# Performance work log

Measured on AMD Instinct MI355X. Metric: run time of the kernel, lower is better.

The kernel has to match this reference:

```python
import jax, jax.numpy as jnp
import numpy as np

D_MODEL = 2048
NUM_HEADS = 16
HEAD_DIM = D_MODEL // NUM_HEADS
EPS = 1e-6


def setup_inputs() -> dict:
    key = jax.random.key(0)
    ks = jax.random.split(key, 5)
    B, S = 1, 4096
    scale = 1.0 / np.sqrt(D_MODEL)
    return {
        "x": jax.random.normal(ks[0], (B, S, D_MODEL), dtype=jnp.float32),
        "wq": jax.random.normal(ks[1], (D_MODEL, D_MODEL), dtype=jnp.float32) * scale,
        "wk": jax.random.normal(ks[2], (D_MODEL, D_MODEL), dtype=jnp.float32) * scale,
        "wv": jax.random.normal(ks[3], (D_MODEL, D_MODEL), dtype=jnp.float32) * scale,
        "wo": jax.random.normal(ks[4], (D_MODEL, D_MODEL), dtype=jnp.float32) * scale,
        "q_norm_w": jnp.ones((HEAD_DIM,), dtype=jnp.float32),
        "k_norm_w": jnp.ones((HEAD_DIM,), dtype=jnp.float32),
    }


def _rmsnorm(x, w):
    rms = jnp.sqrt(jnp.mean(x * x, axis=-1, keepdims=True) + EPS)
    return x / rms * w


def reference(x, wq, wk, wv, wo, q_norm_w, k_norm_w):
    B, S, _ = x.shape
    # nn.Linear: y = x @ W.T ; split heads -> [B, H, S, Dh]
    def proj(w):
        return (x @ w.T).reshape(B, S, NUM_HEADS, HEAD_DIM).transpose(0, 2, 1, 3)
    q = _rmsnorm(proj(wq), q_norm_w)
    k = _rmsnorm(proj(wk), k_norm_w)
    v = proj(wv)
    scale = 1.0 / np.sqrt(HEAD_DIM)
    attn = jnp.einsum("bhqd,bhkd->bhqk", q, k) * scale  # [B,H,S,S]
    attn = jax.nn.softmax(attn, axis=-1)
    out = jnp.einsum("bhqk,bhkd->bhqd", attn, v)
    out = out.transpose(0, 2, 1, 3).reshape(B, S, D_MODEL)
    return out @ wo.T
```

## Files before the change

kernel.cpp:

```cpp
#include <hip/hip_runtime.h>
#include <hip/hip_bf16.h>

#define S 4096
#define D 2048
#define NH 16
#define HD 128

typedef __attribute__((ext_vector_type(8))) short bf16x8;
typedef __attribute__((ext_vector_type(4))) float f32x4;

typedef __attribute__((address_space(1))) char glob_char;
typedef __attribute__((address_space(3))) char lds_char_t;

__device__ __forceinline__ void gld16(const void* g, void* l) {
    __builtin_amdgcn_global_load_lds((const glob_char*)g, (lds_char_t*)l, 16, 0, 0);
}

__device__ __forceinline__ unsigned short f2b(float f) {
    union { float f; unsigned u; } c; c.f = f;
    unsigned r = c.u + 0x7fff + ((c.u >> 16) & 1);
    return (unsigned short)(r >> 16);
}

__device__ __forceinline__ float fexp2(float x) {
#if __has_builtin(__builtin_amdgcn_exp2f)
    return __builtin_amdgcn_exp2f(x);
#else
    return __expf(x * 0.6931471805599453f);
#endif
}

#define MFMA16(a, b, c) __builtin_amdgcn_mfma_f32_16x16x32_bf16((a), (b), (c), 0, 0, 0)

__global__ __launch_bounds__(256) void cvt_all(
    const float* __restrict__ x,  const float* __restrict__ wq,
    const float* __restrict__ wk, const float* __restrict__ wv,
    const float* __restrict__ wo,
    unsigned short* __restrict__ xb, unsigned short* __restrict__ wqkvb,
    unsigned short* __restrict__ wob)
{
    const int z = blockIdx.y;
    const float* src; unsigned short* dst; int n4;
    if (z == 0)      { src = x;  dst = xb;                        n4 = (S * D) / 4; }
    else if (z == 1) { src = wq; dst = wqkvb;                     n4 = (D * D) / 4; }
    else if (z == 2) { src = wk; dst = wqkvb + (size_t)D * D;     n4 = (D * D) / 4; }
    else if (z == 3) { src = wv; dst = wqkvb + 2 * (size_t)D * D; n4 = (D * D) / 4; }
    else             { src = wo; dst = wob;                       n4 = (D * D) / 4; }
    int i = blockIdx.x * 256 + threadIdx.x;
    if (i < n4) {
        float4 v = ((const float4*)src)[i];
        ushort4 o;
        o.x = f2b(v.x); o.y = f2b(v.y); o.z = f2b(v.z); o.w = f2b(v.w);
        ((ushort4*)dst)[i] = o;
    }
}

template<int OUTMODE>
__global__ __launch_bounds__(512, 2) void gemm8(
    const unsigned short* __restrict__ A, const unsigned short* __restrict__ B,
    void* __restrict__ O0, void* __restrict__ O1, void* __restrict__ O2,
    const float* __restrict__ qw, const float* __restrict__ kw)
{
    __shared__ short lds[65536];
    __shared__ float red[4][256];

    const int tid = threadIdx.x;
    const int lane = tid & 63, col = lane & 15, quad = lane >> 4;
    const int w = tid >> 6, wr = w >> 2, wc = w & 3;

    const int nwg = gridDim.x * gridDim.y;
    const int orig = blockIdx.y * gridDim.x + blockIdx.x;
    const int lin = (orig & 7) * (nwg >> 3) + (orig >> 3);
    const int m0 = (lin / gridDim.x) * 256;
    const int n0 = (lin % gridDim.x) * 256;

    const int srow = tid >> 3;
    const int sslot = (tid & 7) ^ (srow & 7);
    const unsigned short* pa0 = A + (size_t)(m0 + srow) * 2048 + sslot * 8;
    const unsigned short* pb0 = B + (size_t)(n0 + srow) * 2048 + sslot * 8;
    const int dst0 = tid * 8;

    auto stA = [&](int t, int h, int buf) {
        const unsigned short* g = pa0 + (size_t)h * 262144 + t * 64;
        short* d = &lds[buf * 16384 + h * 8192 + dst0];
        gld16(g, d);
        gld16(g + 131072, d + 4096);
    };
    auto stB = [&](int t, int h, int buf) {
        const unsigned short* g = pb0 + (size_t)h * 262144 + t * 64;
        short* d = &lds[32768 + buf * 16384 + h * 8192 + dst0];
        gld16(g, d);
        gld16(g + 131072, d + 4096);
    };

    const int sl0 = (quad ^ (col & 7)) << 3;
    const int arow = (wr * 128 + col) * 64;
    const int brow = (wc * 64 + col) * 64;
    auto rdA = [&](int mf, int kk, int buf) -> bf16x8 {
        return *(const bf16x8*)&lds[buf * 16384 + arow + mf * 1024 + (sl0 ^ (kk << 5))];
    };
    auto rdB = [&](int nf, int kk, int buf) -> bf16x8 {
        return *(const bf16x8*)&lds[32768 + buf * 16384 + brow + nf * 1024 + (sl0 ^ (kk << 5))];
    };

    f32x4 acc[8][4];
    #pragma unroll
    for (int i = 0; i < 8; ++i)
        #pragma unroll
        for (int j = 0; j < 4; ++j)
            #pragma unroll
            for (int r = 0; r < 4; ++r) acc[i][j][r] = 0.0f;

    auto ktile = [&](int buf, int tst, int mode) {
        bf16x8 a0[4][2], a1[4][2], b0[2][2], b1[2][2];
        #pragma unroll
        for (int mf = 0; mf < 4; ++mf) { a0[mf][0] = rdA(mf, 0, buf); a0[mf][1] = rdA(mf, 1, buf); }
        #pragma unroll
        for (int nf = 0; nf < 2; ++nf) { b0[nf][0] = rdB(nf, 0, buf); b0[nf][1] = rdB(nf, 1, buf); }
        __builtin_amdgcn_s_barrier();
        __builtin_amdgcn_s_setprio(1);
        #pragma unroll
        for (int mf = 0; mf < 4; ++mf)
            #pragma unroll
            for (int nf = 0; nf < 2; ++nf) {
                acc[mf][nf] = MFMA16(a0[mf][0], b0[nf][0], acc[mf][nf]);
                acc[mf][nf] = MFMA16(a0[mf][1], b0[nf][1], acc[mf][nf]);
            }
        __builtin_amdgcn_s_setprio(0);
        __builtin_amdgcn_s_barrier();

        #pragma unroll
        for (int mf = 0; mf < 4; ++mf) { a1[mf][0] = rdA(mf + 4, 0, buf); a1[mf][1] = rdA(mf + 4, 1, buf); }
        __builtin_amdgcn_s_barrier();
        __builtin_amdgcn_s_setprio(1);
        #pragma unroll
        for (int mf = 0; mf < 4; ++mf)
            #pragma unroll
            for (int nf = 0; nf < 2; ++nf) {
                acc[mf + 4][nf] = MFMA16(a1[mf][0], b0[nf][0], acc[mf + 4][nf]);
                acc[mf + 4][nf] = MFMA16(a1[mf][1], b0[nf][1], acc[mf + 4][nf]);
            }
        __builtin_amdgcn_s_setprio(0);
        __builtin_amdgcn_s_barrier();

        #pragma unroll
        for (int nf = 0; nf < 2; ++nf) { b1[nf][0] = rdB(nf + 2, 0, buf); b1[nf][1] = rdB(nf + 2, 1, buf); }
        if (mode == 0) { stA(tst, 0, buf); stA(tst, 1, buf); }
        __builtin_amdgcn_s_barrier();
        __builtin_amdgcn_s_setprio(1);
        #pragma unroll
        for (int mf = 0; mf < 4; ++mf)
            #pragma unroll
            for (int nf = 0; nf < 2; ++nf) {
                acc[mf][nf + 2] = MFMA16(a0[mf][0], b1[nf][0], acc[mf][nf + 2]);
                acc[mf][nf + 2] = MFMA16(a0[mf][1], b1[nf][1], acc[mf][nf + 2]);
            }
        __builtin_amdgcn_s_setprio(0);
        __builtin_amdgcn_s_barrier();

        if (mode == 0) { stB(tst, 0, buf); stB(tst, 1, buf); }
        __builtin_amdgcn_s_barrier();
        __builtin_amdgcn_s_setprio(1);
        #pragma unroll
        for (int mf = 0; mf < 4; ++mf)
            #pragma unroll
            for (int nf = 0; nf < 2; ++nf) {
                acc[mf + 4][nf + 2] = MFMA16(a1[mf][0], b1[nf][0], acc[mf + 4][nf + 2]);
                acc[mf + 4][nf + 2] = MFMA16(a1[mf][1], b1[nf][1], acc[mf + 4][nf + 2]);
            }
        __builtin_amdgcn_s_setprio(0);
        if (mode == 0)      asm volatile("s_waitcnt vmcnt(8)" ::: "memory");
        else if (mode == 1) asm volatile("s_waitcnt vmcnt(0)" ::: "memory");
        __builtin_amdgcn_s_barrier();
    };

    stA(0, 0, 0); stA(0, 1, 0); stB(0, 0, 0); stB(0, 1, 0);
    stA(1, 0, 1); stA(1, 1, 1); stB(1, 0, 1); stB(1, 1, 1);
    asm volatile("s_waitcnt vmcnt(8)" ::: "memory");
    __builtin_amdgcn_s_barrier();

    for (int kt = 0; kt < 16; ++kt) {
        const int t0 = kt << 1;
        const bool st = kt < 15;
        ktile(0, t0 + 2, st ? 0 : 1);
        ktile(1, t0 + 3, st ? 0 : 2);
    }

    if (OUTMODE == 1) {
        float* C = (float*)O0;
        #pragma unroll
        for (int mf = 0; mf < 8; ++mf)
            #pragma unroll
            for (int nf = 0; nf < 4; ++nf)
                #pragma unroll
                for (int r = 0; r < 4; ++r)
                    C[(size_t)(m0 + wr * 128 + mf * 16 + quad * 4 + r) * 2048 +
                      n0 + wc * 64 + nf * 16 + col] = acc[mf][nf][r];
    } else {
        const int sel = n0 >> 11;
        if (sel == 2) {
            unsigned short* VtO = (unsigned short*)O2;
            #pragma unroll
            for (int mf = 0; mf < 8; ++mf)
                #pragma unroll
                for (int nf = 0; nf < 4; ++nf) {
                    int n = (n0 & 2047) + wc * 64 + nf * 16 + col;
                    int hh = n >> 7, dv = n & 127;
                    ushort4 pk;
                    pk.x = f2b(acc[mf][nf][0]); pk.y = f2b(acc[mf][nf][1]);
                    pk.z = f2b(acc[mf][nf][2]); pk.w = f2b(acc[mf][nf][3]);
                    *(ushort4*)&VtO[(size_t)hh * (HD * S) + (size_t)dv * S +
                                    m0 + wr * 128 + mf * 16 + quad * 4] = pk;
                }
        } else {
            unsigned short* C = (unsigned short*)(sel == 0 ? O0 : O1);
            const float* wgt = (sel == 0) ? qw : kw;
            const float extra = (sel == 0)
                ? 0.08838834764831845f * 1.4426950408889634f : 1.0f;
            float wv4[4];
            #pragma unroll
            for (int nf = 0; nf < 4; ++nf)
                wv4[nf] = wgt[(wc & 1) * 64 + nf * 16 + col];
            #pragma unroll
            for (int mf = 0; mf < 8; ++mf)
                #pragma unroll
                for (int r = 0; r < 4; ++r) {
                    float ss = 0.0f;
                    #pragma unroll
                    for (int nf = 0; nf < 4; ++nf) ss += acc[mf][nf][r] * acc[mf][nf][r];
                    #pragma unroll
                    for (int d = 1; d < 16; d <<= 1) ss += __shfl_xor(ss, d, 64);
                    if (col == 0) red[wc][wr * 128 + mf * 16 + quad * 4 + r] = ss;
                }
            __syncthreads();
            #pragma unroll
            for (int mf = 0; mf < 8; ++mf) {
                float rsc[4];
                #pragma unroll
                for (int r = 0; r < 4; ++r) {
                    int idx = wr * 128 + mf * 16 + quad * 4 + r;
                    float tot = red[wc & 6][idx] + red[(wc & 6) + 1][idx];
                    rsc[r] = rsqrtf(tot * (1.0f / HD) + 1e-6f) * extra;
                }
                #pragma unroll
                for (int nf = 0; nf < 4; ++nf)
                    #pragma unroll
                    for (int r = 0; r < 4; ++r)
                        C[(size_t)(m0 + wr * 128 + mf * 16 + quad * 4 + r) * 2048 +
                          (n0 & 2047) + wc * 64 + nf * 16 + col] =
                            f2b(acc[mf][nf][r] * rsc[r] * wv4[nf]);
            }
        }
    }
}

struct FlashSmem {
    short Ks[2][8192];
    short Vs[2][8192];
    short Ps[8192];
};

__global__ __launch_bounds__(256, 2) void flash_mfma(
    const unsigned short* __restrict__ Qg, const unsigned short* __restrict__ Kg,
    const unsigned short* __restrict__ Vt, unsigned short* __restrict__ Ctx)
{
    __shared__ FlashSmem sm;

    const int tid = threadIdx.x;
    const int w = tid >> 6, lane = tid & 63, col = lane & 15, quad = lane >> 4;
    const int q0 = blockIdx.x * 128, h = blockIdx.y;

    bf16x8 aq[2][4];
    #pragma unroll
    for (int qs = 0; qs < 2; ++qs) {
        const size_t qoff = (size_t)(q0 + w * 32 + qs * 16 + col) * 2048 + h * 128 + quad * 8;
        #pragma unroll
        for (int ds = 0; ds < 4; ++ds)
            aq[qs][ds] = *(const bf16x8*)&Qg[qoff + ds * 32];
    }

    const unsigned short* kga[4];
    const unsigned short* vga[4];
    #pragma unroll
    for (int it = 0; it < 4; ++it) {
        int c = tid + (it << 8);
        {   int ds = c >> 8, rem = c & 255, key = rem >> 2, ch = rem & 3;
            int g = ch ^ ((key >> 1) & 3);
            kga[it] = &Kg[(size_t)key * 2048 + h * 128 + ds * 32 + g * 8]; }
        {   int ks = c >> 9, rem = c & 511, dv = rem >> 2, ch = rem & 3;
            int g = ch ^ ((dv >> 1) & 3);
            vga[it] = &Vt[(size_t)h * (HD * S) + (size_t)dv * S + ks * 32 + g * 8]; }
    }

    const int fb = col * 32 + ((quad ^ ((col >> 1) & 3)) << 3);
    int ap_off[2][2];
    #pragma unroll
    for (int qs = 0; qs < 2; ++qs) {
        int qrow = w * 32 + qs * 16 + col;
        #pragma unroll
        for (int ks = 0; ks < 2; ++ks) {
            int k0 = ks * 32 + quad * 8;
            ap_off[ks][qs] = qrow * 64 + (k0 ^ ((qrow & 7) << 3));
        }
    }
    int psb2[2][4];
    #pragma unroll
    for (int qs = 0; qs < 2; ++qs)
        #pragma unroll
        for (int r = 0; r < 4; ++r) {
            int ql = w * 32 + qs * 16 + quad * 4 + r;
            int s = (ql & 7) << 3;
            psb2[qs][r] = ql * 64 + (col ^ (s & 8)) + (s & 48);
        }

    bf16x8 vone;
    #pragma unroll
    for (int i = 0; i < 8; ++i) vone[i] = (short)0x3F80;

    f32x4 lacc[2];
    f32x4 o[2][8];
    #pragma unroll
    for (int qs = 0; qs < 2; ++qs) {
        #pragma unroll
        for (int r = 0; r < 4; ++r) lacc[qs][r] = 0.0f;
        #pragma unroll
        for (int nj = 0; nj < 8; ++nj)
            #pragma unroll
            for (int r = 0; r < 4; ++r) o[qs][nj][r] = 0.0f;
    }

    auto stage = [&](int b) {
        #pragma unroll
        for (int it = 0; it < 4; ++it) {
            gld16(kga[it], &sm.Ks[b][(tid + (it << 8)) * 8]);
            kga[it] += 64 * 2048;
        }
        #pragma unroll
        for (int it = 0; it < 4; ++it) {
            gld16(vga[it], &sm.Vs[b][(tid + (it << 8)) * 8]);
            vga[it] += 64;
        }
    };

    auto compute = [&](int b) {
        f32x4 sc[2][4];
        #pragma unroll
        for (int qs = 0; qs < 2; ++qs)
            #pragma unroll
            for (int kj = 0; kj < 4; ++kj)
                #pragma unroll
                for (int r = 0; r < 4; ++r) sc[qs][kj][r] = 0.0f;
        __builtin_amdgcn_s_setprio(1);
        #pragma unroll
        for (int ds = 0; ds < 4; ++ds)
            #pragma unroll
            for (int kj = 0; kj < 4; ++kj) {
                bf16x8 bk = *(const bf16x8*)&sm.Ks[b][fb + ds * 2048 + kj * 512];
                sc[0][kj] = MFMA16(aq[0][ds], bk, sc[0][kj]);
                sc[1][kj] = MFMA16(aq[1][ds], bk, sc[1][kj]);
            }
        __builtin_amdgcn_s_setprio(0);

        #pragma unroll
        for (int qs = 0; qs < 2; ++qs)
            #pragma unroll
            for (int kj = 0; kj < 4; ++kj)
                #pragma unroll
                for (int r = 0; r < 4; ++r)
                    sm.Ps[psb2[qs][r] ^ (kj * 16)] = (short)f2b(fexp2(sc[qs][kj][r]));

        __builtin_amdgcn_s_setprio(1);
        #pragma unroll
        for (int ks = 0; ks < 2; ++ks) {
            bf16x8 ap0 = *(const bf16x8*)&sm.Ps[ap_off[ks][0]];
            bf16x8 ap1 = *(const bf16x8*)&sm.Ps[ap_off[ks][1]];
            lacc[0] = MFMA16(ap0, vone, lacc[0]);
            lacc[1] = MFMA16(ap1, vone, lacc[1]);
            #pragma unroll
            for (int nj = 0; nj < 8; ++nj) {
                bf16x8 bv = *(const bf16x8*)&sm.Vs[b][fb + ks * 4096 + nj * 512];
                o[0][nj] = MFMA16(ap0, bv, o[0][nj]);
                o[1][nj] = MFMA16(ap1, bv, o[1][nj]);
            }
        }
        __builtin_amdgcn_s_setprio(0);
    };

    stage(0);
    for (int j0 = 0; j0 < S; j0 += 128) {
        __syncthreads();
        stage(1);
        compute(0);
        __syncthreads();
        if (j0 + 128 < S) stage(0);
        compute(1);
    }

    #pragma unroll
    for (int qs = 0; qs < 2; ++qs) {
        float inv[4];
        #pragma unroll
        for (int r = 0; r < 4; ++r) inv[r] = 1.0f / lacc[qs][r];
        #pragma unroll
        for (int nj = 0; nj < 8; ++nj)
            #pragma unroll
            for (int r = 0; r < 4; ++r)
                Ctx[(size_t)(q0 + w * 32 + qs * 16 + quad * 4 + r) * 2048 + h * 128 + nj * 16 + col] =
                    f2b(o[qs][nj][r] * inv[r]);
    }
}

extern "C" void kernel_launch(void* const* d_in, const int* in_sizes, int n_in,
                              void* d_out, int out_size, void* d_ws, size_t ws_size,
                              hipStream_t stream)
{
    const float* x  = (const float*)d_in[0];
    const float* wq = (const float*)d_in[1];
    const float* wk = (const float*)d_in[2];
    const float* wv = (const float*)d_in[3];
    const float* wo = (const float*)d_in[4];
    const float* qw = (const float*)d_in[5];
    const float* kw = (const float*)d_in[6];
    float* out = (float*)d_out;

    const size_t MB = 1u << 20;
    char* ws = (char*)d_ws;
    unsigned short* xb    = (unsigned short*)(ws);
    unsigned short* Wqkvb = (unsigned short*)(ws + 16 * MB);
    unsigned short* Wob   = (unsigned short*)(ws + 40 * MB);
    unsigned short* Qb    = (unsigned short*)(ws + 48 * MB);
    unsigned short* Kb    = (unsigned short*)(ws + 64 * MB);
    unsigned short* Vt    = (unsigned short*)(ws + 80 * MB);
    unsigned short* Ctx   = xb;

    cvt_all<<<dim3(8192, 5), dim3(256), 0, stream>>>(x, wq, wk, wv, wo, xb, Wqkvb, Wob);

    gemm8<0><<<dim3(24, 16), dim3(512), 0, stream>>>(xb, Wqkvb, Qb, Kb, Vt, qw, kw);

    flash_mfma<<<dim3(32, 16), dim3(256), 0, stream>>>(Qb, Kb, Vt, Ctx);

    gemm8<1><<<dim3(8, 16), dim3(512), 0, stream>>>(Ctx, Wob, out, out, out, qw, kw);
}
```

Baseline: 459.6 us.

## Keep softmax probabilities in registers via lane shuffles instead of LDS round-trip

The QK^T MFMA operands are swapped so the score tile comes out transposed, with keys along rows. The exponentiated probabilities are then packed to bf16 pairs and redistributed across lanes with shuffles to form the A-operand fragments for the PV MFMA. This removes the Ps shared-memory buffer along with its scattered 2-byte stores and vector reloads, and frees LDS. In exchange it adds many cross-lane shuffle instructions and selects, and may raise register pressure.

```diff
diff --git a/kernel.cpp b/kernel.cpp
--- a/kernel.cpp
+++ b/kernel.cpp
@@ -28,6 +28,16 @@
 #else
     return __expf(x * 0.6931471805599453f);
 #endif
+}
+
+__device__ __forceinline__ unsigned pk2(float a, float b) {
+    return (unsigned)f2b(a) | ((unsigned)f2b(b) << 16);
+}
+
+__device__ __forceinline__ bf16x8 mkfrag(unsigned a, unsigned b, unsigned c, unsigned d) {
+    union { unsigned u[4]; bf16x8 v; } x;
+    x.u[0] = a; x.u[1] = b; x.u[2] = c; x.u[3] = d;
+    return x.v;
 }
 
 #define MFMA16(a, b, c) __builtin_amdgcn_mfma_f32_16x16x32_bf16((a), (b), (c), 0, 0, 0)
@@ -257,7 +267,6 @@
 struct FlashSmem {
     short Ks[2][8192];
     short Vs[2][8192];
-    short Ps[8192];
 };
 
 __global__ __launch_bounds__(256, 2) void flash_mfma(
@@ -293,25 +302,7 @@
     }
 
     const int fb = col * 32 + ((quad ^ ((col >> 1) & 3)) << 3);
-    int ap_off[2][2];
-    #pragma unroll
-    for (int qs = 0; qs < 2; ++qs) {
-        int qrow = w * 32 + qs * 16 + col;
-        #pragma unroll
-        for (int ks = 0; ks < 2; ++ks) {
-            int k0 = ks * 32 + quad * 8;
-            ap_off[ks][qs] = qrow * 64 + (k0 ^ ((qrow & 7) << 3));
-        }
-    }
-    int psb2[2][4];
-    #pragma unroll
-    for (int qs = 0; qs < 2; ++qs)
-        #pragma unroll
-        for (int r = 0; r < 4; ++r) {
-            int ql = w * 32 + qs * 16 + quad * 4 + r;
-            int s = (ql & 7) << 3;
-            psb2[qs][r] = ql * 64 + (col ^ (s & 8)) + (s & 48);
-        }
+    const int src0 = col + 32 * (quad & 1);
 
     bf16x8 vone;
     #pragma unroll
@@ -356,8 +347,8 @@
             #pragma unroll
             for (int kj = 0; kj < 4; ++kj) {
                 bf16x8 bk = *(const bf16x8*)&sm.Ks[b][fb + ds * 2048 + kj * 512];
-                sc[0][kj] = MFMA16(aq[0][ds], bk, sc[0][kj]);
-                sc[1][kj] = MFMA16(aq[1][ds], bk, sc[1][kj]);
+                sc[0][kj] = MFMA16(bk, aq[0][ds], sc[0][kj]);
+                sc[1][kj] = MFMA16(bk, aq[1][ds], sc[1][kj]);
             }
         __builtin_amdgcn_s_setprio(0);
 
@@ -367,20 +358,52 @@
             for (int kj = 0; kj < 4; ++kj)
                 #pragma unroll
                 for (int r = 0; r < 4; ++r)
-                    sm.Ps[psb2[qs][r] ^ (kj * 16)] = (short)f2b(fexp2(sc[qs][kj][r]));
+                    sc[qs][kj][r] = fexp2(sc[qs][kj][r]);
+
+        unsigned wp[2][4][2];
+        #pragma unroll
+        for (int qs = 0; qs < 2; ++qs)
+            #pragma unroll
+            for (int kj = 0; kj < 4; ++kj)
+                #pragma unroll
+                for (int hh = 0; hh < 2; ++hh)
+                    wp[qs][kj][hh] = pk2(sc[qs][kj][2 * hh], sc[qs][kj][2 * hh + 1]);
+
+        unsigned apw[2][2][4];
+        #pragma unroll
+        for (int qs = 0; qs < 2; ++qs)
+            #pragma unroll
+            for (int g = 0; g < 2; ++g) {
+                const int srcl = src0 + 16 * g;
+                #pragma unroll
+                for (int hh = 0; hh < 2; ++hh) {
+                    unsigned t0 = (unsigned)__shfl((int)wp[qs][0][hh], srcl, 64);
+                    unsigned t1 = (unsigned)__shfl((int)wp[qs][1][hh], srcl, 64);
+                    unsigned t2 = (unsigned)__shfl((int)wp[qs][2][hh], srcl, 64);
+                    unsigned t3 = (unsigned)__shfl((int)wp[qs][3][hh], srcl, 64);
+                    const int j2 = 2 * g + hh;
+                    apw[qs][0][j2] = (quad & 2) ? t1 : t0;
+                    apw[qs][1][j2] = (quad & 2) ? t3 : t2;
+                }
+            }
+        bf16x8 ap[2][2];
+        #pragma unroll
+        for (int qs = 0; qs < 2; ++qs)
+            #pragma unroll
+            for (int ks = 0; ks < 2; ++ks)
+                ap[qs][ks] = mkfrag(apw[qs][ks][0], apw[qs][ks][1],
+                                    apw[qs][ks][2], apw[qs][ks][3]);
 
         __builtin_amdgcn_s_setprio(1);
         #pragma unroll
         for (int ks = 0; ks < 2; ++ks) {
-            bf16x8 ap0 = *(const bf16x8*)&sm.Ps[ap_off[ks][0]];
-            bf16x8 ap1 = *(const bf16x8*)&sm.Ps[ap_off[ks][1]];
-            lacc[0] = MFMA16(ap0, vone, lacc[0]);
-            lacc[1] = MFMA16(ap1, vone, lacc[1]);
+            lacc[0] = MFMA16(ap[0][ks], vone, lacc[0]);
+            lacc[1] = MFMA16(ap[1][ks], vone, lacc[1]);
             #pragma unroll
             for (int nj = 0; nj < 8; ++nj) {
                 bf16x8 bv = *(const bf16x8*)&sm.Vs[b][fb + ks * 4096 + nj * 512];
-                o[0][nj] = MFMA16(ap0, bv, o[0][nj]);
-                o[1][nj] = MFMA16(ap1, bv, o[1][nj]);
+                o[0][nj] = MFMA16(ap[0][ks], bv, o[0][nj]);
+                o[1][nj] = MFMA16(ap[1][ks], bv, o[1][nj]);
             }
         }
         __builtin_amdgcn_s_setprio(0);
```

Measured after the change: 475.4 us. +3.4%, slower.
